# Kernel optimization log

Measured on AMD Instinct MI355X. Metric: run time of the kernel, lower is better.

The kernel has to match this reference:

```python
import jax, jax.numpy as jnp
import numpy as np

P_DROP = 0.6  # F.dropout default training=True in the original forward

def setup_inputs() -> dict:
    key = jax.random.key(0)
    k1, k2, k3, k4 = jax.random.split(key, 4)
    B, T, V, F, K, O = 32, 12, 1000, 64, 3, 64
    x = jax.random.normal(k1, (B, T, V, F), dtype=jnp.float32)
    Att = jax.random.uniform(k2, (V, V), dtype=jnp.float32)
    cheb = jax.random.normal(k3, (K, V, V), dtype=jnp.float32)   # Chebyshev polynomials T_k(L)
    Theta = jax.random.normal(k4, (K, F, O), dtype=jnp.float32)  # per-order feature transforms
    return {"x": x, "Att": Att, "cheb": cheb, "Theta": Theta}

def reference(x, Att, cheb, Theta):
    # x: [B,T,V,F]; Att: [V,V]; cheb: [K,V,V]; Theta: [K,F,O]
    B, T, V, F = x.shape
    K = cheb.shape[0]
    keep = 1.0 - P_DROP
    # Original draws a fresh dropout mask per (time_step, k); replicate with a fixed key.
    mask = jax.random.bernoulli(jax.random.key(42), keep, (T, K, V, V))
    TkA = cheb * Att                                   # [K,V,V] attention-weighted polynomial
    M = jnp.where(mask, TkA[None] / keep, 0.0)         # [T,K,V,V] inverted dropout
    # rhs = T_k_with_at @ graph_signal, batched over (b,t,k)
    rhs = jnp.einsum('tkuv,btvf->btkuf', M, x)         # [B,T,K,V,F]
    # sum_k rhs_k @ Theta_k  -> [B,T,V,O]; matches permute(0,3,1,2) of stacked outputs
    out = jnp.einsum('btkuf,kfo->btuo', rhs, Theta)
    return jax.nn.relu(out)
```

## Files before the change

### kernel.cpp

```cpp
#include <hip/hip_runtime.h>
#include <hip/hip_bf16.h>
#include <stdint.h>


typedef __attribute__((ext_vector_type(8))) short short8;
typedef __attribute__((ext_vector_type(4))) float f32x4;

#define MASK_VARIANT 0

__device__ __forceinline__ ushort f2bf(float f) {
  __hip_bfloat16 h = __float2bfloat16(f);
  return *reinterpret_cast<ushort*>(&h);
}

__device__ __forceinline__ void threefry2x32(uint32_t c0, uint32_t c1,
                                             uint32_t& o0, uint32_t& o1) {
  const uint32_t ks0 = 0u;
  const uint32_t ks1 = 42u;
  const uint32_t ks2 = ks0 ^ ks1 ^ 0x1BD11BDAu;
  uint32_t x0 = c0 + ks0;
  uint32_t x1 = c1 + ks1;
#define TFR(r) { x0 += x1; x1 = (x1 << (r)) | (x1 >> (32 - (r))); x1 ^= x0; }
  TFR(13) TFR(15) TFR(26) TFR(6)
  x0 += ks1; x1 += ks2 + 1u;
  TFR(17) TFR(29) TFR(16) TFR(24)
  x0 += ks2; x1 += ks0 + 2u;
  TFR(13) TFR(15) TFR(26) TFR(6)
  x0 += ks0; x1 += ks1 + 3u;
  TFR(17) TFR(29) TFR(16) TFR(24)
  x0 += ks1; x1 += ks2 + 4u;
  TFR(13) TFR(15) TFR(26) TFR(6)
  x0 += ks2; x1 += ks0 + 5u;
#undef TFR
  o0 = x0; o1 = x1;
}

__global__ void build_m(const float* __restrict__ Att,
                        const float* __restrict__ cheb,
                        ushort* __restrict__ Mws) {
  const uint32_t idx = blockIdx.x * 256u + threadIdx.x;
  const uint32_t vp = idx & 1023u;
  const uint32_t up = (idx >> 10) & 1023u;
  const uint32_t tk = idx >> 20;
  float val = 0.f;
  if ((vp < 1000u) & (up < 1000u)) {
    const uint32_t flat = (tk * 1000u + up) * 1000u + vp;
    uint32_t o0, o1, bits;
#if MASK_VARIANT == 3
    if (flat < 18000000u) { threefry2x32(flat, flat + 18000000u, o0, o1); bits = o0; }
    else                  { threefry2x32(flat - 18000000u, flat, o0, o1); bits = o1; }
#else
    threefry2x32(0u, flat, o0, o1);
#if MASK_VARIANT == 0
    bits = o0 ^ o1;
#elif MASK_VARIANT == 1
    bits = o1;
#else
    bits = o0;
#endif
#endif
    const float u = __uint_as_float((bits >> 9) | 0x3f800000u) - 1.0f;
    if (u < 0.4f) {
      val = cheb[(tk % 3u) * 1000000u + up * 1000u + vp] *
            Att[up * 1000u + vp] * 2.5f;
    }
  }
  Mws[idx] = f2bf(val);
}

__global__ void transpose_x(const float* __restrict__ x,
                            ushort* __restrict__ xt) {
  __shared__ float lt[64][65];
  const int vc = blockIdx.x, t = blockIdx.y, b = blockIdx.z;
  const int tid = threadIdx.x;
  const int v0 = vc * 64;
#pragma unroll
  for (int i = 0; i < 4; ++i) {
    const int c = i * 256 + tid;
    const int vi = c >> 4, f4 = c & 15;
    float4 q = make_float4(0.f, 0.f, 0.f, 0.f);
    if (v0 + vi < 1000)
      q = *(const float4*)(x + ((((size_t)b * 12 + t) * 1000 + v0 + vi) << 6) + f4 * 4);
    lt[f4 * 4 + 0][vi] = q.x;
    lt[f4 * 4 + 1][vi] = q.y;
    lt[f4 * 4 + 2][vi] = q.z;
    lt[f4 * 4 + 3][vi] = q.w;
  }
  __syncthreads();
  const int f = tid >> 2, g = tid & 3;
  alignas(16) ushort tmp[16];
#pragma unroll
  for (int j = 0; j < 16; ++j) tmp[j] = f2bf(lt[f][g * 16 + j]);
  const size_t base = ((size_t)(t * 2048 + b * 64 + f)) << 10;
  *(uint4*)(xt + base + v0 + g * 16)     = *(const uint4*)&tmp[0];
  *(uint4*)(xt + base + v0 + g * 16 + 8) = *(const uint4*)&tmp[8];
}

#define LDP 72

__device__ __forceinline__ f32x4 mfma_bf16(short8 a, short8 b, f32x4 c) {
  asm volatile("v_mfma_f32_16x16x32_bf16 %0, %1, %2, %0"
               : "+v"(c) : "v"(a), "v"(b));
  return c;
}

__global__ __launch_bounds__(256, 2)
void cheb_main(const ushort* __restrict__ Mws, const ushort* __restrict__ xt,
               const float* __restrict__ Theta, float* __restrict__ out) {
  __shared__ ushort sAB[2 * 128 * LDP];
  __shared__ ushort sTh[3 * 64 * LDP];

  const int tid = threadIdx.x;
  const int lane = tid & 63;
  const int w = tid >> 6;
  const int wu = w >> 1, wn = w & 1;
  const int quad = lane >> 4, l15 = lane & 15;
  const int nt = blockIdx.x, ut = blockIdx.y, t = blockIdx.z;
  const int u0 = ut * 128, n0 = nt * 128;

  for (int e = tid; e < 3 * 64 * 64; e += 256) {
    const int kk = e >> 12, rem = e & 4095, f = rem >> 6, o = rem & 63;
    sTh[kk * (64 * LDP) + o * LDP + f] = f2bf(Theta[e]);
  }

  f32x4 oacc[4][4];
#pragma unroll
  for (int i = 0; i < 4; ++i)
#pragma unroll
    for (int j = 0; j < 4; ++j) oacc[i][j] = f32x4{0.f, 0.f, 0.f, 0.f};

  ushort* sA = sAB;
  ushort* sB = sAB + 128 * LDP;
  ushort* sP = sAB + w * (64 * LDP);

  for (int kk = 0; kk < 3; ++kk) {
    f32x4 pacc[4][4];
#pragma unroll
    for (int i = 0; i < 4; ++i)
#pragma unroll
      for (int j = 0; j < 4; ++j) pacc[i][j] = f32x4{0.f, 0.f, 0.f, 0.f};

    const size_t mbase = (size_t)(t * 3 + kk) << 20;

    for (int vc = 0; vc < 16; ++vc) {
      __syncthreads();
#pragma unroll
      for (int i = 0; i < 4; ++i) {
        const int c = i * 256 + tid;
        const int row = c >> 3, seg = c & 7;
        const int col = vc * 64 + seg * 8;
        const uint4 va = *(const uint4*)(Mws + mbase + ((size_t)(u0 + row) << 10) + col);
        *(uint4*)&sA[row * LDP + seg * 8] = va;
        const uint4 vb = *(const uint4*)(xt + (((size_t)(t * 2048 + n0 + row)) << 10) + col);
        *(uint4*)&sB[row * LDP + seg * 8] = vb;
      }
      __syncthreads();
#pragma unroll
      for (int ks = 0; ks < 2; ++ks) {
        short8 av[4], bv[4];
#pragma unroll
        for (int mi = 0; mi < 4; ++mi)
          av[mi] = *(const short8*)&sA[(wu * 64 + mi * 16 + l15) * LDP + ks * 32 + quad * 8];
#pragma unroll
        for (int ni = 0; ni < 4; ++ni)
          bv[ni] = *(const short8*)&sB[(wn * 64 + ni * 16 + l15) * LDP + ks * 32 + quad * 8];
#pragma unroll
        for (int mi = 0; mi < 4; ++mi)
#pragma unroll
          for (int ni = 0; ni < 4; ++ni)
            pacc[mi][ni] = mfma_bf16(av[mi], bv[ni], pacc[mi][ni]);
      }
    }

    __syncthreads();
#pragma unroll
    for (int mi = 0; mi < 4; ++mi)
#pragma unroll
      for (int ni = 0; ni < 4; ++ni)
#pragma unroll
        for (int r = 0; r < 4; ++r)
          sP[(mi * 16 + quad * 4 + r) * LDP + ni * 16 + l15] = f2bf(pacc[mi][ni][r]);
    __syncthreads();
#pragma unroll
    for (int ks = 0; ks < 2; ++ks) {
      short8 a2[4], b2[4];
#pragma unroll
      for (int mi = 0; mi < 4; ++mi)
        a2[mi] = *(const short8*)&sP[(mi * 16 + l15) * LDP + ks * 32 + quad * 8];
#pragma unroll
      for (int ni = 0; ni < 4; ++ni)
        b2[ni] = *(const short8*)&sTh[kk * (64 * LDP) + (ni * 16 + l15) * LDP + ks * 32 + quad * 8];
#pragma unroll
      for (int mi = 0; mi < 4; ++mi)
#pragma unroll
        for (int ni = 0; ni < 4; ++ni)
          oacc[mi][ni] = mfma_bf16(a2[mi], b2[ni], oacc[mi][ni]);
    }
  }

#pragma unroll
  for (int mi = 0; mi < 4; ++mi) {
    const int u_base = u0 + wu * 64 + mi * 16 + quad * 4;
#pragma unroll
    for (int ni = 0; ni < 4; ++ni) {
      const int n = n0 + wn * 64 + ni * 16 + l15;
      const int b = n >> 6, oo = n & 63;
      float* op = out + (((size_t)b * 12 + t) * 1000) * 64 + oo;
#pragma unroll
      for (int r = 0; r < 4; ++r) {
        const int u = u_base + r;
        if (u < 1000) op[(size_t)u * 64] = fmaxf(oacc[mi][ni][r], 0.f);
      }
    }
  }
}

extern "C" void kernel_launch(void* const* d_in, const int* in_sizes, int n_in,
                              void* d_out, int out_size, void* d_ws, size_t ws_size,
                              hipStream_t stream) {
  const float* x     = (const float*)d_in[0];
  const float* Att   = (const float*)d_in[1];
  const float* cheb  = (const float*)d_in[2];
  const float* Theta = (const float*)d_in[3];
  float* out = (float*)d_out;

  ushort* Mws = (ushort*)d_ws;
  ushort* xtw = Mws + 37748736ull;

  build_m<<<147456, 256, 0, stream>>>(Att, cheb, Mws);
  transpose_x<<<dim3(16, 12, 32), 256, 0, stream>>>(x, xtw);
  cheb_main<<<dim3(16, 8, 12), 256, 0, stream>>>(Mws, xtw, Theta, out);
}
```

Measured before the change: 315.2 us.

## Use 512-thread blocks with XOR-swizzled LDS tiles and per-k Theta staging

The main GEMM kernel now runs 8 waves per block, each owning a 32x64 tile instead of 64x64, which halves per-wave accumulators so more waves can be resident. The A/B tiles are stored unpadded with an XOR chunk swizzle to avoid LDS bank conflicts. Theta is staged one order at a time into a smaller LDS region instead of all three at once. Shared memory per block shrinks. The costs are extra barriers, a reload of Theta on each k, and less register-level reuse per wave. The mask-variant macros are also removed.

```diff
diff --git a/kernel.cpp b/kernel.cpp
--- a/kernel.cpp
+++ b/kernel.cpp
@@ -5,8 +5,6 @@
 
 typedef __attribute__((ext_vector_type(8))) short short8;
 typedef __attribute__((ext_vector_type(4))) float f32x4;
-
-#define MASK_VARIANT 0
 
 __device__ __forceinline__ ushort f2bf(float f) {
   __hip_bfloat16 h = __float2bfloat16(f);
@@ -45,20 +43,9 @@
   float val = 0.f;
   if ((vp < 1000u) & (up < 1000u)) {
     const uint32_t flat = (tk * 1000u + up) * 1000u + vp;
-    uint32_t o0, o1, bits;
-#if MASK_VARIANT == 3
-    if (flat < 18000000u) { threefry2x32(flat, flat + 18000000u, o0, o1); bits = o0; }
-    else                  { threefry2x32(flat - 18000000u, flat, o0, o1); bits = o1; }
-#else
+    uint32_t o0, o1;
     threefry2x32(0u, flat, o0, o1);
-#if MASK_VARIANT == 0
-    bits = o0 ^ o1;
-#elif MASK_VARIANT == 1
-    bits = o1;
-#else
-    bits = o0;
-#endif
-#endif
+    const uint32_t bits = o0 ^ o1;
     const float u = __uint_as_float((bits >> 9) | 0x3f800000u) - 1.0f;
     if (u < 0.4f) {
       val = cheb[(tk % 3u) * 1000000u + up * 1000u + vp] *
@@ -96,7 +83,7 @@
   *(uint4*)(xt + base + v0 + g * 16 + 8) = *(const uint4*)&tmp[8];
 }
 
-#define LDP 72
+#define LDT 72
 
 __device__ __forceinline__ f32x4 mfma_bf16(short8 a, short8 b, f32x4 c) {
   asm volatile("v_mfma_f32_16x16x32_bf16 %0, %1, %2, %0"
@@ -104,12 +91,10 @@
   return c;
 }
 
-__global__ __launch_bounds__(256, 2)
+__global__ __launch_bounds__(512, 3)
 void cheb_main(const ushort* __restrict__ Mws, const ushort* __restrict__ xt,
                const float* __restrict__ Theta, float* __restrict__ out) {
-  __shared__ ushort sAB[2 * 128 * LDP];
-  __shared__ ushort sTh[3 * 64 * LDP];
-
+  __shared__ __align__(16) ushort smem[23040];
   const int tid = threadIdx.x;
   const int lane = tid & 63;
   const int w = tid >> 6;
@@ -118,54 +103,68 @@
   const int nt = blockIdx.x, ut = blockIdx.y, t = blockIdx.z;
   const int u0 = ut * 128, n0 = nt * 128;
 
-  for (int e = tid; e < 3 * 64 * 64; e += 256) {
-    const int kk = e >> 12, rem = e & 4095, f = rem >> 6, o = rem & 63;
-    sTh[kk * (64 * LDP) + o * LDP + f] = f2bf(Theta[e]);
-  }
-
-  f32x4 oacc[4][4];
-#pragma unroll
-  for (int i = 0; i < 4; ++i)
+  ushort* sA  = smem;
+  ushort* sB  = smem + 8192;
+  ushort* sP  = smem + w * (32 * LDT);
+  ushort* sTh = smem + 8 * 32 * LDT;
+
+  const int srow = lane >> 3;
+  const int schunk = lane & 7;
+  const int gchunk = schunk ^ srow;
+  const int rsw = l15 & 7;
+
+  f32x4 oacc[2][4];
+#pragma unroll
+  for (int i = 0; i < 2; ++i)
 #pragma unroll
     for (int j = 0; j < 4; ++j) oacc[i][j] = f32x4{0.f, 0.f, 0.f, 0.f};
 
-  ushort* sA = sAB;
-  ushort* sB = sAB + 128 * LDP;
-  ushort* sP = sAB + w * (64 * LDP);
-
   for (int kk = 0; kk < 3; ++kk) {
-    f32x4 pacc[4][4];
-#pragma unroll
-    for (int i = 0; i < 4; ++i)
+    __syncthreads();
+    for (int e = tid; e < 4096; e += 512) {
+      const int f = e >> 6, o = e & 63;
+      sTh[o * LDT + f] = f2bf(Theta[kk * 4096 + e]);
+    }
+
+    f32x4 pacc[2][4];
+#pragma unroll
+    for (int i = 0; i < 2; ++i)
 #pragma unroll
       for (int j = 0; j < 4; ++j) pacc[i][j] = f32x4{0.f, 0.f, 0.f, 0.f};
 
     const size_t mbase = (size_t)(t * 3 + kk) << 20;
+    const size_t xrow0 = (size_t)(t * 2048 + n0);
 
     for (int vc = 0; vc < 16; ++vc) {
       __syncthreads();
 #pragma unroll
-      for (int i = 0; i < 4; ++i) {
-        const int c = i * 256 + tid;
-        const int row = c >> 3, seg = c & 7;
-        const int col = vc * 64 + seg * 8;
-        const uint4 va = *(const uint4*)(Mws + mbase + ((size_t)(u0 + row) << 10) + col);
-        *(uint4*)&sA[row * LDP + seg * 8] = va;
-        const uint4 vb = *(const uint4*)(xt + (((size_t)(t * 2048 + n0 + row)) << 10) + col);
-        *(uint4*)&sB[row * LDP + seg * 8] = vb;
+      for (int j = 0; j < 2; ++j) {
+        const int rr = 8 * (w * 2 + j) + srow;
+        const uint4 va = *(const uint4*)(Mws + mbase +
+                          ((size_t)(u0 + rr) << 10) + vc * 64 + gchunk * 8);
+        *(uint4*)&sA[(w * 2 + j) * 512 + lane * 8] = va;
+        const uint4 vb = *(const uint4*)(xt +
+                          ((xrow0 + rr) << 10) + vc * 64 + gchunk * 8);
+        *(uint4*)&sB[(w * 2 + j) * 512 + lane * 8] = vb;
       }
       __syncthreads();
 #pragma unroll
       for (int ks = 0; ks < 2; ++ks) {
-        short8 av[4], bv[4];
-#pragma unroll
-        for (int mi = 0; mi < 4; ++mi)
-          av[mi] = *(const short8*)&sA[(wu * 64 + mi * 16 + l15) * LDP + ks * 32 + quad * 8];
-#pragma unroll
-        for (int ni = 0; ni < 4; ++ni)
-          bv[ni] = *(const short8*)&sB[(wn * 64 + ni * 16 + l15) * LDP + ks * 32 + quad * 8];
-#pragma unroll
-        for (int mi = 0; mi < 4; ++mi)
+        short8 av[2], bv[4];
+#pragma unroll
+        for (int mi = 0; mi < 2; ++mi) {
+          const int row = wu * 32 + mi * 16 + l15;
+          const int c = (ks * 4 + quad) ^ rsw;
+          av[mi] = *(const short8*)&sA[row * 64 + c * 8];
+        }
+#pragma unroll
+        for (int ni = 0; ni < 4; ++ni) {
+          const int row = wn * 64 + ni * 16 + l15;
+          const int c = (ks * 4 + quad) ^ rsw;
+          bv[ni] = *(const short8*)&sB[row * 64 + c * 8];
+        }
+#pragma unroll
+        for (int mi = 0; mi < 2; ++mi)
 #pragma unroll
           for (int ni = 0; ni < 4; ++ni)
             pacc[mi][ni] = mfma_bf16(av[mi], bv[ni], pacc[mi][ni]);
@@ -174,24 +173,24 @@
 
     __syncthreads();
 #pragma unroll
-    for (int mi = 0; mi < 4; ++mi)
+    for (int mi = 0; mi < 2; ++mi)
 #pragma unroll
       for (int ni = 0; ni < 4; ++ni)
 #pragma unroll
         for (int r = 0; r < 4; ++r)
-          sP[(mi * 16 + quad * 4 + r) * LDP + ni * 16 + l15] = f2bf(pacc[mi][ni][r]);
+          sP[(mi * 16 + quad * 4 + r) * LDT + ni * 16 + l15] = f2bf(pacc[mi][ni][r]);
     __syncthreads();
 #pragma unroll
     for (int ks = 0; ks < 2; ++ks) {
-      short8 a2[4], b2[4];
-#pragma unroll
-      for (int mi = 0; mi < 4; ++mi)
-        a2[mi] = *(const short8*)&sP[(mi * 16 + l15) * LDP + ks * 32 + quad * 8];
+      short8 a2[2], b2[4];
+#pragma unroll
+      for (int mi = 0; mi < 2; ++mi)
+        a2[mi] = *(const short8*)&sP[(mi * 16 + l15) * LDT + ks * 32 + quad * 8];
 #pragma unroll
       for (int ni = 0; ni < 4; ++ni)
-        b2[ni] = *(const short8*)&sTh[kk * (64 * LDP) + (ni * 16 + l15) * LDP + ks * 32 + quad * 8];
-#pragma unroll
-      for (int mi = 0; mi < 4; ++mi)
+        b2[ni] = *(const short8*)&sTh[(ni * 16 + l15) * LDT + ks * 32 + quad * 8];
+#pragma unroll
+      for (int mi = 0; mi < 2; ++mi)
 #pragma unroll
         for (int ni = 0; ni < 4; ++ni)
           oacc[mi][ni] = mfma_bf16(a2[mi], b2[ni], oacc[mi][ni]);
@@ -199,8 +198,8 @@
   }
 
 #pragma unroll
-  for (int mi = 0; mi < 4; ++mi) {
-    const int u_base = u0 + wu * 64 + mi * 16 + quad * 4;
+  for (int mi = 0; mi < 2; ++mi) {
+    const int u_base = u0 + wu * 32 + mi * 16 + quad * 4;
 #pragma unroll
     for (int ni = 0; ni < 4; ++ni) {
       const int n = n0 + wn * 64 + ni * 16 + l15;
@@ -229,5 +228,5 @@
 
   build_m<<<147456, 256, 0, stream>>>(Att, cheb, Mws);
   transpose_x<<<dim3(16, 12, 32), 256, 0, stream>>>(x, xtw);
-  cheb_main<<<dim3(16, 8, 12), 256, 0, stream>>>(Mws, xtw, Theta, out);
-}
+  cheb_main<<<dim3(16, 8, 12), 512, 0, stream>>>(Mws, xtw, Theta, out);
+}
```

Measured after the change: 310.7 us. About the same (-1.4%).
